# Performance work log

Measured on AMD Instinct MI355X. Metric: run time of the kernel, lower is better.

The kernel has to match this reference:

```python
import jax, jax.numpy as jnp
import numpy as np

BN_EPS = 1e-5

def conv1x1(x, w, b):
    # x: [B,C,H,W], w: [O,C], b: [O] -> [B,O,H,W]
    return jnp.einsum('bchw,oc->bohw', x, w) + b[None, :, None, None]

def setup_inputs() -> dict:
    key = jax.random.key(0)
    ks = jax.random.split(key, 12)
    B, C, H, W = 16, 256, 64, 32
    Ci = C // 2  # reduc_ratio = 2
    s_in = 1.0 / np.sqrt(C)
    s_ci = 1.0 / np.sqrt(Ci)
    return {
        'x':        jax.random.normal(ks[0], (B, C, H, W), jnp.float32),
        'w_theta':  jax.random.normal(ks[1], (Ci, C), jnp.float32) * s_in,
        'b_theta':  jax.random.normal(ks[2], (Ci,), jnp.float32) * 0.01,
        'w_phi':    jax.random.normal(ks[3], (Ci, C), jnp.float32) * s_in,
        'b_phi':    jax.random.normal(ks[4], (Ci,), jnp.float32) * 0.01,
        'w_g':      jax.random.normal(ks[5], (Ci, C), jnp.float32) * s_in,
        'b_g':      jax.random.normal(ks[6], (Ci,), jnp.float32) * 0.01,
        'w_out':    jax.random.normal(ks[7], (C, Ci), jnp.float32) * s_ci,
        'b_out':    jax.random.normal(ks[8], (C,), jnp.float32) * 0.01,
        'gamma':    jax.random.normal(ks[9], (C,), jnp.float32) * 0.1 + 1.0,
        'beta':     jax.random.normal(ks[10], (C,), jnp.float32) * 0.1,
        'run_mean': jax.random.normal(ks[11], (C,), jnp.float32) * 0.1,
        'run_var':  jax.random.uniform(jax.random.fold_in(key, 99), (C,), jnp.float32, 0.5, 1.5),
    }

def reference(x, w_theta, b_theta, w_phi, b_phi, w_g, b_g, w_out, b_out,
              gamma, beta, run_mean, run_var):
    B, C, H, W = x.shape
    Ci = w_theta.shape[0]
    N = H * W
    theta = conv1x1(x, w_theta, b_theta).reshape(B, Ci, N)  # [B,Ci,N]
    phi   = conv1x1(x, w_phi,   b_phi  ).reshape(B, Ci, N)  # [B,Ci,N]
    g     = conv1x1(x, w_g,     b_g    ).reshape(B, Ci, N)  # [B,Ci,N]
    # f = theta^T @ phi, normalized by N (no softmax)
    f = jnp.einsum('bcn,bcm->bnm', theta, phi) / N           # [B,N,N]
    # y = f @ g^T, back to channel-first layout
    y = jnp.einsum('bnm,bcm->bcn', f, g).reshape(B, Ci, H, W)
    w_y = conv1x1(y, w_out, b_out)                           # [B,C,H,W]
    inv = gamma / jnp.sqrt(run_var + BN_EPS)
    bn = w_y * inv[None, :, None, None] + (beta - run_mean * inv)[None, :, None, None]
    return bn + x
```

## Files before the change

kernel.cpp:

```cpp
#include <hip/hip_runtime.h>
#include <cstddef>
#include <cstdint>

typedef unsigned short ushort_t;
typedef short short8 __attribute__((ext_vector_type(8)));
typedef float f32x4 __attribute__((ext_vector_type(4)));

#define BB 16
#define CC 256
#define CI 128
#define NN 2048
#define BN_EPS 1e-5f
#define NCH 4

#define OFF_EH    0u
#define OFF_WGT   16384u
#define OFF_WFT   32768u
#define OFF_WTT   49152u
#define OFF_LH    65536u
#define OFF_RT    98304u
#define OFF_Q     131072u
#define OFF_W1    131328u
#define OFF_EG    131584u
#define OFF_BB2   131840u
#define OFF_BFBT  132096u
#define OFF_S     132112u
#define OFF_V1    136208u
#define OFF_V2    140304u
#define OFF_SQ    144400u
#define OFF_BIASP 144416u
#define OFF_GH    148512u
#define OFF_TH    672800u
#define OFF_PH    1197088u
#define OFF_XH    1721376u
#define OFF_XHT   5915680u
#define OFF_GP    10109984u
#define WS_FLOATS 14304288u

__device__ __forceinline__ ushort_t f2bf(float f) {
  unsigned int u = __float_as_uint(f);
  u += 0x7fffu + ((u >> 16) & 1u);
  return (ushort_t)(u >> 16);
}
__device__ __forceinline__ float bf2f(ushort_t h) {
  return __uint_as_float((unsigned int)h << 16);
}

__device__ __forceinline__ void gl_lds16(const void* gsrc, void* ldst) {
  __builtin_amdgcn_global_load_lds(
      (const __attribute__((address_space(1))) void*)gsrc,
      (__attribute__((address_space(3))) void*)ldst, 16, 0, 0);
}

__device__ __forceinline__ void mfma_core(
    const ushort_t* gA, size_t ldA, const ushort_t* gB, size_t ldB,
    int kIters, ushort_t* ldsA, ushort_t* ldsB, f32x4 acc[4][4]) {
  const int t = threadIdx.x;
  const int wave = t >> 6, lane = t & 63;
  const int wm = wave & 1, wn = wave >> 1;
  const int l15 = lane & 15, lhi = lane >> 4;

  for (int kt = 0; kt < kIters; ++kt) {
#pragma unroll
    for (int q = 0; q < 4; ++q) {
      int row = wave * 32 + q * 8 + (lane >> 3);
      int gs = (lane & 7) ^ (row & 7);
      gl_lds16(gA + (size_t)row * ldA + gs * 8, &ldsA[(wave * 4 + q) * 512]);
    }
#pragma unroll
    for (int q = 0; q < 4; ++q) {
      int row = wave * 32 + q * 8 + (lane >> 3);
      int gs = (lane & 7) ^ (row & 7);
      gl_lds16(gB + (size_t)row * ldB + gs * 8, &ldsB[(wave * 4 + q) * 512]);
    }
    __syncthreads();
#pragma unroll
    for (int ks = 0; ks < 2; ++ks) {
      short8 af[4], bf[4];
#pragma unroll
      for (int i = 0; i < 4; ++i) {
        int rowA = wm * 64 + i * 16 + l15;
        int grA = (4 * ks + lhi) ^ (rowA & 7);
        af[i] = *(const short8*)&ldsA[rowA * 64 + grA * 8];
        int rowB = wn * 64 + i * 16 + l15;
        int grB = (4 * ks + lhi) ^ (rowB & 7);
        bf[i] = *(const short8*)&ldsB[rowB * 64 + grB * 8];
      }
#pragma unroll
      for (int i = 0; i < 4; ++i)
#pragma unroll
        for (int j = 0; j < 4; ++j)
          acc[i][j] = __builtin_amdgcn_mfma_f32_16x16x32_bf16(
              af[i], bf[j], acc[i][j], 0, 0, 0);
    }
    __syncthreads();
    gA += 64; gB += 64;
  }
}

#define ACC_INIT(acc) \
  _Pragma("unroll") for (int i_ = 0; i_ < 4; ++i_) \
  _Pragma("unroll") for (int j_ = 0; j_ < 4; ++j_) \
  _Pragma("unroll") for (int e_ = 0; e_ < 4; ++e_) acc[i_][j_][e_] = 0.f;

__device__ __forceinline__ void store_bf16_D(
    f32x4 acc[4][4], ushort_t* D, int ldd, int m0, int n0) {
  int t = threadIdx.x, wave = t >> 6, lane = t & 63;
  int wm = wave & 1, wn = wave >> 1, l15 = lane & 15, lhi = lane >> 4;
#pragma unroll
  for (int i = 0; i < 4; ++i)
#pragma unroll
    for (int j = 0; j < 4; ++j)
#pragma unroll
      for (int r = 0; r < 4; ++r) {
        int a = m0 + wm * 64 + i * 16 + 4 * lhi + r;
        int bc = n0 + wn * 64 + j * 16 + l15;
        D[(size_t)a * ldd + bc] = f2bf(acc[i][j][r]);
      }
}

__global__ __launch_bounds__(256) void pack(
    const float* __restrict__ wg, const float* __restrict__ wp,
    const float* __restrict__ wt, const float* __restrict__ wout,
    const float* __restrict__ gamma, const float* __restrict__ run_var,
    const float* __restrict__ b_out, const float* __restrict__ beta,
    const float* __restrict__ run_mean,
    ushort_t* __restrict__ Eh, ushort_t* __restrict__ WgT,
    ushort_t* __restrict__ WfT, ushort_t* __restrict__ WtT,
    float* __restrict__ bias2) {
  int gid = blockIdx.x * 256 + threadIdx.x;
  if (gid < 4 * 32768) {
    int which = gid >> 15, idx = gid & 32767;
    int c = idx >> 7, j = idx & 127;
    if (which == 0) {
      float inv = gamma[c] * rsqrtf(run_var[c] + BN_EPS);
      Eh[idx] = f2bf(inv * (1.0f / (float)NN) * wout[idx]);
    } else {
      const float* src = (which == 1) ? wg : (which == 2) ? wp : wt;
      ushort_t* dst = (which == 1) ? WgT : (which == 2) ? WfT : WtT;
      dst[idx] = f2bf(src[(size_t)j * CC + c]);
    }
  } else if (gid < 4 * 32768 + CC) {
    int o = gid - 4 * 32768;
    float inv = gamma[o] * rsqrtf(run_var[o] + BN_EPS);
    bias2[o] = b_out[o] * inv + beta[o] - run_mean[o] * inv;
  }
}

__global__ __launch_bounds__(256) void pack2(
    const float* __restrict__ wp, const float* __restrict__ wt,
    const float* __restrict__ wout, const float* __restrict__ bt,
    const float* __restrict__ bp, const float* __restrict__ bg,
    const float* __restrict__ gamma, const float* __restrict__ run_var,
    float* __restrict__ q, float* __restrict__ w1, float* __restrict__ eg,
    float* __restrict__ bfbt) {
  int t = threadIdx.x;
  float aq = 0.f, aw = 0.f;
  for (int j = 0; j < CI; ++j) {
    aq += wp[(size_t)j * CC + t] * bt[j];
    aw += wt[(size_t)j * CC + t] * bp[j];
  }
  q[t] = aq; w1[t] = aw;
  float inv = gamma[t] * rsqrtf(run_var[t] + BN_EPS);
  float s2 = 0.f;
  for (int i = 0; i < CI; ++i) s2 += wout[(size_t)t * CI + i] * bg[i];
  eg[t] = inv * (1.0f / (float)NN) * s2;
  if (t == 0) {
    float d = 0.f;
    for (int j = 0; j < CI; ++j) d += bp[j] * bt[j];
    *bfbt = d;
  }
}

__global__ __launch_bounds__(256) void cast_x(
    const float* __restrict__ x, ushort_t* __restrict__ xhT,
    ushort_t* __restrict__ xh, float* __restrict__ s) {
  __shared__ float Xs[64][65];
  int n0 = blockIdx.x * 64, c0 = blockIdx.y * 64, b = blockIdx.z;
  int t = threadIdx.x;
  int tr = t >> 4, tc = (t & 15) * 4;
#pragma unroll
  for (int p = 0; p < 4; ++p) {
    int row = p * 16 + tr;
    float4 v = *(const float4*)&x[((size_t)b * CC + c0 + row) * NN + n0 + tc];
    Xs[row][tc] = v.x; Xs[row][tc + 1] = v.y; Xs[row][tc + 2] = v.z; Xs[row][tc + 3] = v.w;
  }
  __syncthreads();
#pragma unroll
  for (int p = 0; p < 4; ++p) {
    int j = p * 16 + tr;
    ushort4 hv;
    hv.x = f2bf(Xs[tc][j]); hv.y = f2bf(Xs[tc + 1][j]);
    hv.z = f2bf(Xs[tc + 2][j]); hv.w = f2bf(Xs[tc + 3][j]);
    *(ushort4*)&xhT[((size_t)b * NN + n0 + j) * CC + c0 + tc] = hv;
  }
  {
    int row = t >> 2, cg = (t & 3) * 16;
    size_t base = ((size_t)b * CC + c0 + row) * NN + n0 + cg;
#pragma unroll
    for (int e = 0; e < 4; ++e) {
      ushort4 hv;
      hv.x = f2bf(Xs[row][cg + 4 * e]);     hv.y = f2bf(Xs[row][cg + 4 * e + 1]);
      hv.z = f2bf(Xs[row][cg + 4 * e + 2]); hv.w = f2bf(Xs[row][cg + 4 * e + 3]);
      *(ushort4*)&xh[base + 4 * e] = hv;
    }
  }
  if (t < 64) {
    float p = 0.f;
    for (int j2 = 0; j2 < 64; ++j2) p += Xs[t][j2];
    atomicAdd(&s[(size_t)b * CC + c0 + t], p);
  }
}

__global__ __launch_bounds__(256) void gemm_k128(
    const ushort_t* __restrict__ A, const ushort_t* __restrict__ B,
    ushort_t* __restrict__ D) {
  __shared__ __align__(16) ushort_t As[8192], Bs[8192];
  int n0 = blockIdx.x * 128, m0 = blockIdx.y * 128;
  f32x4 acc[4][4]; ACC_INIT(acc);
  mfma_core(A + (size_t)m0 * 128, 128, B + (size_t)n0 * 128, 128, 2, As, Bs, acc);
  store_bf16_D(acc, D, CC, m0, n0);
}

__global__ __launch_bounds__(256) void k_G(
    const ushort_t* __restrict__ xh, float* __restrict__ G_part) {
  __shared__ __align__(16) ushort_t As[8192], Bs[8192];
  int ch = blockIdx.x, ij = blockIdx.y, b = blockIdx.z;
  int ti = ij >> 1, tj = ij & 1;
  f32x4 acc[4][4]; ACC_INIT(acc);
  mfma_core(xh + ((size_t)b * CC + ti * 128) * NN + ch * (NN / NCH), NN,
            xh + ((size_t)b * CC + tj * 128) * NN + ch * (NN / NCH), NN,
            (NN / NCH) / 64, As, Bs, acc);
  float* dst = G_part + ((size_t)ch * BB + b) * (CC * CC);
  int t = threadIdx.x, wave = t >> 6, lane = t & 63;
  int wm = wave & 1, wn = wave >> 1, l15 = lane & 15, lhi = lane >> 4;
#pragma unroll
  for (int i = 0; i < 4; ++i)
#pragma unroll
    for (int j = 0; j < 4; ++j)
#pragma unroll
      for (int r = 0; r < 4; ++r) {
        int a = ti * 128 + wm * 64 + i * 16 + 4 * lhi + r;
        int bc = tj * 128 + wn * 64 + j * 16 + l15;
        dst[(size_t)a * CC + bc] = acc[i][j][r];
      }
}

__global__ __launch_bounds__(256) void g_red(
    const float* __restrict__ G_part, ushort_t* __restrict__ Gh) {
  int b = blockIdx.y;
  int e = blockIdx.x * 256 + threadIdx.x;
  float v = 0.f;
#pragma unroll
  for (int c = 0; c < NCH; ++c)
    v += G_part[((size_t)c * BB + b) * (CC * CC) + e];
  Gh[(size_t)b * (CC * CC) + e] = f2bf(v);
}

__global__ __launch_bounds__(256) void k_s(
    const ushort_t* __restrict__ Lh, const ushort_t* __restrict__ Rt,
    const float* __restrict__ s, const float* __restrict__ q,
    float* __restrict__ v1, float* __restrict__ v2, float* __restrict__ sq) {
  __shared__ float sl[256], red[256];
  int b = blockIdx.x, t = threadIdx.x;
  sl[t] = s[(size_t)b * CC + t];
  __syncthreads();
  float a1 = 0.f, a2 = 0.f;
  for (int c = 0; c < CC; ++c) {
    a1 += bf2f(Lh[(size_t)t * CC + c]) * sl[c];
    a2 += bf2f(Rt[(size_t)t * CC + c]) * sl[c];
  }
  v1[(size_t)b * CC + t] = a1;
  v2[(size_t)b * CC + t] = a2;
  red[t] = sl[t] * q[t];
  __syncthreads();
  for (int st = 128; st > 0; st >>= 1) {
    if (t < st) red[t] += red[t + st];
    __syncthreads();
  }
  if (t == 0) sq[b] = red[0];
}

__global__ __launch_bounds__(256) void c1(
    const ushort_t* __restrict__ Lh, const ushort_t* __restrict__ Gh,
    ushort_t* __restrict__ Th) {
  __shared__ __align__(16) ushort_t As[8192], Bs[8192];
  int n0 = blockIdx.x * 128, m0 = blockIdx.y * 128, b = blockIdx.z;
  f32x4 acc[4][4]; ACC_INIT(acc);
  mfma_core(Lh + (size_t)m0 * CC, CC,
            Gh + (size_t)b * (CC * CC) + (size_t)n0 * CC, CC, 4, As, Bs, acc);
  store_bf16_D(acc, Th + (size_t)b * (CC * CC), CC, m0, n0);
}

__global__ __launch_bounds__(256) void c2(
    const ushort_t* __restrict__ Th, const ushort_t* __restrict__ Rt,
    const float* __restrict__ v1, const float* __restrict__ v2,
    const float* __restrict__ eg, const float* __restrict__ w1,
    ushort_t* __restrict__ Ph) {
  __shared__ __align__(16) ushort_t As[8192], Bs[8192];
  int n0 = blockIdx.x * 128, m0 = blockIdx.y * 128, b = blockIdx.z;
  f32x4 acc[4][4]; ACC_INIT(acc);
  mfma_core(Th + (size_t)b * (CC * CC) + (size_t)m0 * CC, CC,
            Rt + (size_t)n0 * CC, CC, 4, As, Bs, acc);
  ushort_t* D = Ph + (size_t)b * (CC * CC);
  int t = threadIdx.x, wave = t >> 6, lane = t & 63;
  int wm = wave & 1, wn = wave >> 1, l15 = lane & 15, lhi = lane >> 4;
#pragma unroll
  for (int i = 0; i < 4; ++i)
#pragma unroll
    for (int r = 0; r < 4; ++r) {
      int o = m0 + wm * 64 + i * 16 + 4 * lhi + r;
      float vo = v1[(size_t)b * CC + o] + (float)NN * eg[o];
      float eo = eg[o];
#pragma unroll
      for (int j = 0; j < 4; ++j) {
        int c = n0 + wn * 64 + j * 16 + l15;
        float val = acc[i][j][r] + eo * v2[(size_t)b * CC + c] + vo * w1[c];
        D[(size_t)o * CC + c] = f2bf(val);
      }
    }
}

__global__ __launch_bounds__(256) void k_bias(
    const ushort_t* __restrict__ Th, const float* __restrict__ q,
    const float* __restrict__ eg, const float* __restrict__ v1,
    const float* __restrict__ sq, const float* __restrict__ bfbt,
    const float* __restrict__ bias2, float* __restrict__ biasp) {
  int b = blockIdx.x, o = threadIdx.x;
  const ushort_t* Trow = Th + (size_t)b * (CC * CC) + (size_t)o * CC;
  float a = 0.f;
  for (int k = 0; k < CC; ++k) a += bf2f(Trow[k]) * q[k];
  biasp[(size_t)b * CC + o] =
      a + eg[o] * sq[b] + (v1[(size_t)b * CC + o] + (float)NN * eg[o]) * (*bfbt)
      + bias2[o];
}

__global__ __launch_bounds__(256) void k_out(
    const ushort_t* __restrict__ Ph, const ushort_t* __restrict__ xhT,
    const float* __restrict__ biasp, const float* __restrict__ x,
    float* __restrict__ out) {
  __shared__ __align__(16) ushort_t As[8192], Bs[8192];
  int n0 = blockIdx.x * 128, o0 = blockIdx.y * 128, b = blockIdx.z;
  f32x4 acc[4][4]; ACC_INIT(acc);
  mfma_core(Ph + (size_t)b * (CC * CC) + (size_t)o0 * CC, CC,
            xhT + ((size_t)b * NN + n0) * CC, CC, 4, As, Bs, acc);
  int t = threadIdx.x, wave = t >> 6, lane = t & 63;
  int wm = wave & 1, wn = wave >> 1, l15 = lane & 15, lhi = lane >> 4;
#pragma unroll
  for (int i = 0; i < 4; ++i)
#pragma unroll
    for (int r = 0; r < 4; ++r) {
      int o = o0 + wm * 64 + i * 16 + 4 * lhi + r;
      float bo = biasp[(size_t)b * CC + o];
#pragma unroll
      for (int j = 0; j < 4; ++j) {
        int n = n0 + wn * 64 + j * 16 + l15;
        size_t idx = ((size_t)b * CC + o) * NN + n;
        out[idx] = acc[i][j][r] + bo + x[idx];
      }
    }
}

extern "C" void kernel_launch(void* const* d_in, const int* in_sizes, int n_in,
                              void* d_out, int out_size, void* d_ws, size_t ws_size,
                              hipStream_t stream) {
  const float* x        = (const float*)d_in[0];
  const float* w_theta  = (const float*)d_in[1];
  const float* b_theta  = (const float*)d_in[2];
  const float* w_phi    = (const float*)d_in[3];
  const float* b_phi    = (const float*)d_in[4];
  const float* w_g      = (const float*)d_in[5];
  const float* b_g      = (const float*)d_in[6];
  const float* w_out    = (const float*)d_in[7];
  const float* b_out    = (const float*)d_in[8];
  const float* gamma    = (const float*)d_in[9];
  const float* beta     = (const float*)d_in[10];
  const float* run_mean = (const float*)d_in[11];
  const float* run_var  = (const float*)d_in[12];
  float* out = (float*)d_out;
  float* ws  = (float*)d_ws;

  if (ws_size < (size_t)WS_FLOATS * sizeof(float)) return;

  ushort_t* Eh   = (ushort_t*)(ws + OFF_EH);
  ushort_t* WgT  = (ushort_t*)(ws + OFF_WGT);
  ushort_t* WfT  = (ushort_t*)(ws + OFF_WFT);
  ushort_t* WtT  = (ushort_t*)(ws + OFF_WTT);
  ushort_t* Lh   = (ushort_t*)(ws + OFF_LH);
  ushort_t* Rt   = (ushort_t*)(ws + OFF_RT);
  float*    q    = ws + OFF_Q;
  float*    w1   = ws + OFF_W1;
  float*    eg   = ws + OFF_EG;
  float*    bias2= ws + OFF_BB2;
  float*    bfbt = ws + OFF_BFBT;
  float*    s    = ws + OFF_S;
  float*    v1   = ws + OFF_V1;
  float*    v2   = ws + OFF_V2;
  float*    sq   = ws + OFF_SQ;
  float*    biasp= ws + OFF_BIASP;
  ushort_t* Gh   = (ushort_t*)(ws + OFF_GH);
  ushort_t* Th   = (ushort_t*)(ws + OFF_TH);
  ushort_t* Ph   = (ushort_t*)(ws + OFF_PH);
  ushort_t* xh   = (ushort_t*)(ws + OFF_XH);
  ushort_t* xhT  = (ushort_t*)(ws + OFF_XHT);
  float*    Gp   = ws + OFF_GP;

  pack<<<dim3(513), 256, 0, stream>>>(w_g, w_phi, w_theta, w_out, gamma, run_var,
                                      b_out, beta, run_mean, Eh, WgT, WfT, WtT, bias2);
  pack2<<<dim3(1), 256, 0, stream>>>(w_phi, w_theta, w_out, b_theta, b_phi, b_g,
                                     gamma, run_var, q, w1, eg, bfbt);
  hipMemsetAsync(s, 0, (size_t)BB * CC * sizeof(float), stream);
  cast_x<<<dim3(NN / 64, CC / 64, BB), 256, 0, stream>>>(x, xhT, xh, s);
  gemm_k128<<<dim3(2, 2), 256, 0, stream>>>(Eh, WgT, Lh);
  gemm_k128<<<dim3(2, 2), 256, 0, stream>>>(WtT, WfT, Rt);
  k_G<<<dim3(NCH, 4, BB), 256, 0, stream>>>(xh, Gp);
  g_red<<<dim3(CC * CC / 256, BB), 256, 0, stream>>>(Gp, Gh);
  k_s<<<dim3(BB), 256, 0, stream>>>(Lh, Rt, s, q, v1, v2, sq);
  c1<<<dim3(2, 2, BB), 256, 0, stream>>>(Lh, Gh, Th);
  c2<<<dim3(2, 2, BB), 256, 0, stream>>>(Th, Rt, v1, v2, eg, w1, Ph);
  k_bias<<<dim3(BB), 256, 0, stream>>>(Th, q, eg, v1, sq, bfbt, bias2, biasp);
  k_out<<<dim3(NN / 128, CC / 128, BB), 256, 0, stream>>>(Ph, xhT, biasp, x, out);
}
```

Baseline: 207.1 us.

## Fuse prep and per-batch chain kernels, drop split-K, read bf16 residual

New measurement: 266.0 us. +28.4%, slower.

```diff
diff --git a/kernel.cpp b/kernel.cpp
--- a/kernel.cpp
+++ b/kernel.cpp
@@ -11,31 +11,22 @@
 #define CI 128
 #define NN 2048
 #define BN_EPS 1e-5f
-#define NCH 4
-
-#define OFF_EH    0u
-#define OFF_WGT   16384u
-#define OFF_WFT   32768u
-#define OFF_WTT   49152u
-#define OFF_LH    65536u
-#define OFF_RT    98304u
-#define OFF_Q     131072u
-#define OFF_W1    131328u
-#define OFF_EG    131584u
-#define OFF_BB2   131840u
-#define OFF_BFBT  132096u
-#define OFF_S     132112u
-#define OFF_V1    136208u
-#define OFF_V2    140304u
-#define OFF_SQ    144400u
-#define OFF_BIASP 144416u
-#define OFF_GH    148512u
-#define OFF_TH    672800u
-#define OFF_PH    1197088u
-#define OFF_XH    1721376u
-#define OFF_XHT   5915680u
-#define OFF_GP    10109984u
-#define WS_FLOATS 14304288u
+
+#define OFF_LH    0u
+#define OFF_RT    32768u
+#define OFF_Q     65536u
+#define OFF_W1    65792u
+#define OFF_EG    66048u
+#define OFF_BB2   66304u
+#define OFF_BFBT  66560u
+#define OFF_BIASP 66576u
+#define OFF_SS    70672u
+#define OFF_GH    74768u
+#define OFF_TH    599056u
+#define OFF_PH    1123344u
+#define OFF_XH    1647632u
+#define OFF_XHT   5841936u
+#define WS_FLOATS 10036240u
 
 __device__ __forceinline__ ushort_t f2bf(float f) {
   unsigned int u = __float_as_uint(f);
@@ -119,56 +110,68 @@
       }
 }
 
-__global__ __launch_bounds__(256) void pack(
-    const float* __restrict__ wg, const float* __restrict__ wp,
-    const float* __restrict__ wt, const float* __restrict__ wout,
-    const float* __restrict__ gamma, const float* __restrict__ run_var,
-    const float* __restrict__ b_out, const float* __restrict__ beta,
-    const float* __restrict__ run_mean,
-    ushort_t* __restrict__ Eh, ushort_t* __restrict__ WgT,
-    ushort_t* __restrict__ WfT, ushort_t* __restrict__ WtT,
-    float* __restrict__ bias2) {
-  int gid = blockIdx.x * 256 + threadIdx.x;
-  if (gid < 4 * 32768) {
-    int which = gid >> 15, idx = gid & 32767;
-    int c = idx >> 7, j = idx & 127;
-    if (which == 0) {
-      float inv = gamma[c] * rsqrtf(run_var[c] + BN_EPS);
-      Eh[idx] = f2bf(inv * (1.0f / (float)NN) * wout[idx]);
-    } else {
-      const float* src = (which == 1) ? wg : (which == 2) ? wp : wt;
-      ushort_t* dst = (which == 1) ? WgT : (which == 2) ? WfT : WtT;
-      dst[idx] = f2bf(src[(size_t)j * CC + c]);
-    }
-  } else if (gid < 4 * 32768 + CC) {
-    int o = gid - 4 * 32768;
-    float inv = gamma[o] * rsqrtf(run_var[o] + BN_EPS);
-    bias2[o] = b_out[o] * inv + beta[o] - run_mean[o] * inv;
-  }
-}
-
-__global__ __launch_bounds__(256) void pack2(
-    const float* __restrict__ wp, const float* __restrict__ wt,
-    const float* __restrict__ wout, const float* __restrict__ bt,
-    const float* __restrict__ bp, const float* __restrict__ bg,
-    const float* __restrict__ gamma, const float* __restrict__ run_var,
+__global__ __launch_bounds__(256) void prep(
+    const float* __restrict__ wt, const float* __restrict__ wp,
+    const float* __restrict__ wg, const float* __restrict__ wout,
+    const float* __restrict__ bt, const float* __restrict__ bp,
+    const float* __restrict__ bg, const float* __restrict__ gamma,
+    const float* __restrict__ beta, const float* __restrict__ run_mean,
+    const float* __restrict__ run_var, const float* __restrict__ b_out,
+    ushort_t* __restrict__ Lh, ushort_t* __restrict__ Rt,
     float* __restrict__ q, float* __restrict__ w1, float* __restrict__ eg,
-    float* __restrict__ bfbt) {
-  int t = threadIdx.x;
-  float aq = 0.f, aw = 0.f;
-  for (int j = 0; j < CI; ++j) {
-    aq += wp[(size_t)j * CC + t] * bt[j];
-    aw += wt[(size_t)j * CC + t] * bp[j];
-  }
-  q[t] = aq; w1[t] = aw;
-  float inv = gamma[t] * rsqrtf(run_var[t] + BN_EPS);
-  float s2 = 0.f;
-  for (int i = 0; i < CI; ++i) s2 += wout[(size_t)t * CI + i] * bg[i];
-  eg[t] = inv * (1.0f / (float)NN) * s2;
-  if (t == 0) {
-    float d = 0.f;
-    for (int j = 0; j < CI; ++j) d += bp[j] * bt[j];
-    *bfbt = d;
+    float* __restrict__ bias2, float* __restrict__ bfbt,
+    float* __restrict__ s) {
+  int blk = blockIdx.x, t = threadIdx.x;
+  if (blk < 16) {
+    int o = blk * 16 + (t >> 4);
+    int j0 = (t & 15) * 16;
+    float inv = gamma[o] * rsqrtf(run_var[o] + BN_EPS) * (1.0f / (float)NN);
+    float acc[16];
+#pragma unroll
+    for (int e = 0; e < 16; ++e) acc[e] = 0.f;
+    for (int k = 0; k < CI; ++k) {
+      float a = wout[(size_t)o * CI + k];
+      const float* wgr = &wg[(size_t)k * CC + j0];
+#pragma unroll
+      for (int e = 0; e < 16; ++e) acc[e] += a * wgr[e];
+    }
+#pragma unroll
+    for (int e = 0; e < 16; ++e)
+      Lh[(size_t)o * CC + j0 + e] = f2bf(inv * acc[e]);
+  } else if (blk < 32) {
+    int a = (blk - 16) * 16 + (t >> 4);
+    int b0 = (t & 15) * 16;
+    float acc[16];
+#pragma unroll
+    for (int e = 0; e < 16; ++e) acc[e] = 0.f;
+    for (int j = 0; j < CI; ++j) {
+      float av = wt[(size_t)j * CC + a];
+      const float* wpr = &wp[(size_t)j * CC + b0];
+#pragma unroll
+      for (int e = 0; e < 16; ++e) acc[e] += av * wpr[e];
+    }
+#pragma unroll
+    for (int e = 0; e < 16; ++e)
+      Rt[(size_t)a * CC + b0 + e] = f2bf(acc[e]);
+  } else {
+    float aq = 0.f, aw = 0.f;
+    for (int j = 0; j < CI; ++j) {
+      aq += wp[(size_t)j * CC + t] * bt[j];
+      aw += wt[(size_t)j * CC + t] * bp[j];
+    }
+    q[t] = aq; w1[t] = aw;
+    float inv = gamma[t] * rsqrtf(run_var[t] + BN_EPS);
+    float s2 = 0.f;
+    for (int i = 0; i < CI; ++i) s2 += wout[(size_t)t * CI + i] * bg[i];
+    eg[t] = inv * (1.0f / (float)NN) * s2;
+    bias2[t] = b_out[t] * inv + beta[t] - run_mean[t] * inv;
+    if (t == 0) {
+      float d = 0.f;
+      for (int j = 0; j < CI; ++j) d += bp[j] * bt[j];
+      *bfbt = d;
+    }
+#pragma unroll
+    for (int i = 0; i < BB; ++i) s[(size_t)i * CC + t] = 0.f;
   }
 }
 
@@ -212,137 +215,121 @@
   }
 }
 
-__global__ __launch_bounds__(256) void gemm_k128(
-    const ushort_t* __restrict__ A, const ushort_t* __restrict__ B,
-    ushort_t* __restrict__ D) {
+__global__ __launch_bounds__(256) void k_G(
+    const ushort_t* __restrict__ xh, ushort_t* __restrict__ Gh_all) {
   __shared__ __align__(16) ushort_t As[8192], Bs[8192];
-  int n0 = blockIdx.x * 128, m0 = blockIdx.y * 128;
-  f32x4 acc[4][4]; ACC_INIT(acc);
-  mfma_core(A + (size_t)m0 * 128, 128, B + (size_t)n0 * 128, 128, 2, As, Bs, acc);
-  store_bf16_D(acc, D, CC, m0, n0);
-}
-
-__global__ __launch_bounds__(256) void k_G(
-    const ushort_t* __restrict__ xh, float* __restrict__ G_part) {
-  __shared__ __align__(16) ushort_t As[8192], Bs[8192];
-  int ch = blockIdx.x, ij = blockIdx.y, b = blockIdx.z;
+  int ij = blockIdx.x, b = blockIdx.y;
   int ti = ij >> 1, tj = ij & 1;
   f32x4 acc[4][4]; ACC_INIT(acc);
-  mfma_core(xh + ((size_t)b * CC + ti * 128) * NN + ch * (NN / NCH), NN,
-            xh + ((size_t)b * CC + tj * 128) * NN + ch * (NN / NCH), NN,
-            (NN / NCH) / 64, As, Bs, acc);
-  float* dst = G_part + ((size_t)ch * BB + b) * (CC * CC);
-  int t = threadIdx.x, wave = t >> 6, lane = t & 63;
-  int wm = wave & 1, wn = wave >> 1, l15 = lane & 15, lhi = lane >> 4;
-#pragma unroll
-  for (int i = 0; i < 4; ++i)
-#pragma unroll
-    for (int j = 0; j < 4; ++j)
-#pragma unroll
-      for (int r = 0; r < 4; ++r) {
-        int a = ti * 128 + wm * 64 + i * 16 + 4 * lhi + r;
-        int bc = tj * 128 + wn * 64 + j * 16 + l15;
-        dst[(size_t)a * CC + bc] = acc[i][j][r];
-      }
-}
-
-__global__ __launch_bounds__(256) void g_red(
-    const float* __restrict__ G_part, ushort_t* __restrict__ Gh) {
-  int b = blockIdx.y;
-  int e = blockIdx.x * 256 + threadIdx.x;
-  float v = 0.f;
-#pragma unroll
-  for (int c = 0; c < NCH; ++c)
-    v += G_part[((size_t)c * BB + b) * (CC * CC) + e];
-  Gh[(size_t)b * (CC * CC) + e] = f2bf(v);
-}
-
-__global__ __launch_bounds__(256) void k_s(
-    const ushort_t* __restrict__ Lh, const ushort_t* __restrict__ Rt,
-    const float* __restrict__ s, const float* __restrict__ q,
-    float* __restrict__ v1, float* __restrict__ v2, float* __restrict__ sq) {
-  __shared__ float sl[256], red[256];
+  mfma_core(xh + ((size_t)b * CC + ti * 128) * NN, NN,
+            xh + ((size_t)b * CC + tj * 128) * NN, NN, NN / 64, As, Bs, acc);
+  store_bf16_D(acc, Gh_all + (size_t)b * (CC * CC), CC, ti * 128, tj * 128);
+}
+
+__global__ __launch_bounds__(256) void k_cc(
+    const float* __restrict__ s, const ushort_t* __restrict__ Lh,
+    const ushort_t* __restrict__ Rt, const ushort_t* __restrict__ Gh_all,
+    ushort_t* __restrict__ Th_all, ushort_t* __restrict__ Ph_all,
+    const float* __restrict__ q, const float* __restrict__ w1,
+    const float* __restrict__ eg, const float* __restrict__ bias2,
+    const float* __restrict__ bfbt, float* __restrict__ biasp) {
+  __shared__ __align__(16) ushort_t As[8192], Bs[8192];
+  __shared__ float sl[256], v1l[256], v2l[256], red[256];
+  __shared__ float ql[256], egl[256], w1l[256];
+  __shared__ float sql;
   int b = blockIdx.x, t = threadIdx.x;
+  const ushort_t* Gh = Gh_all + (size_t)b * (CC * CC);
+  ushort_t* Th = Th_all + (size_t)b * (CC * CC);
+  ushort_t* Ph = Ph_all + (size_t)b * (CC * CC);
+
   sl[t] = s[(size_t)b * CC + t];
-  __syncthreads();
-  float a1 = 0.f, a2 = 0.f;
-  for (int c = 0; c < CC; ++c) {
-    a1 += bf2f(Lh[(size_t)t * CC + c]) * sl[c];
-    a2 += bf2f(Rt[(size_t)t * CC + c]) * sl[c];
-  }
-  v1[(size_t)b * CC + t] = a1;
-  v2[(size_t)b * CC + t] = a2;
-  red[t] = sl[t] * q[t];
+  ql[t] = q[t]; egl[t] = eg[t]; w1l[t] = w1[t];
+  __syncthreads();
+
+  {
+    int rl = t >> 4, ch = t & 15;
+    for (int pass = 0; pass < 16; ++pass) {
+      int o = pass * 16 + rl;
+      float a1 = 0.f, a2 = 0.f;
+#pragma unroll
+      for (int e = 0; e < 16; ++e) {
+        float sv = sl[ch * 16 + e];
+        a1 += bf2f(Lh[(size_t)o * CC + ch * 16 + e]) * sv;
+        a2 += bf2f(Rt[(size_t)o * CC + ch * 16 + e]) * sv;
+      }
+#pragma unroll
+      for (int w = 8; w >= 1; w >>= 1) {
+        a1 += __shfl_xor(a1, w, 16);
+        a2 += __shfl_xor(a2, w, 16);
+      }
+      if (ch == 0) { v1l[o] = a1; v2l[o] = a2; }
+    }
+    red[t] = sl[t] * ql[t];
+  }
   __syncthreads();
   for (int st = 128; st > 0; st >>= 1) {
     if (t < st) red[t] += red[t + st];
     __syncthreads();
   }
-  if (t == 0) sq[b] = red[0];
-}
-
-__global__ __launch_bounds__(256) void c1(
-    const ushort_t* __restrict__ Lh, const ushort_t* __restrict__ Gh,
-    ushort_t* __restrict__ Th) {
-  __shared__ __align__(16) ushort_t As[8192], Bs[8192];
-  int n0 = blockIdx.x * 128, m0 = blockIdx.y * 128, b = blockIdx.z;
-  f32x4 acc[4][4]; ACC_INIT(acc);
-  mfma_core(Lh + (size_t)m0 * CC, CC,
-            Gh + (size_t)b * (CC * CC) + (size_t)n0 * CC, CC, 4, As, Bs, acc);
-  store_bf16_D(acc, Th + (size_t)b * (CC * CC), CC, m0, n0);
-}
-
-__global__ __launch_bounds__(256) void c2(
-    const ushort_t* __restrict__ Th, const ushort_t* __restrict__ Rt,
-    const float* __restrict__ v1, const float* __restrict__ v2,
-    const float* __restrict__ eg, const float* __restrict__ w1,
-    ushort_t* __restrict__ Ph) {
-  __shared__ __align__(16) ushort_t As[8192], Bs[8192];
-  int n0 = blockIdx.x * 128, m0 = blockIdx.y * 128, b = blockIdx.z;
-  f32x4 acc[4][4]; ACC_INIT(acc);
-  mfma_core(Th + (size_t)b * (CC * CC) + (size_t)m0 * CC, CC,
-            Rt + (size_t)n0 * CC, CC, 4, As, Bs, acc);
-  ushort_t* D = Ph + (size_t)b * (CC * CC);
-  int t = threadIdx.x, wave = t >> 6, lane = t & 63;
+  if (t == 0) sql = red[0];
+  __syncthreads();
+
+  for (int m0 = 0; m0 < CC; m0 += 128)
+    for (int n0 = 0; n0 < CC; n0 += 128) {
+      f32x4 acc[4][4]; ACC_INIT(acc);
+      mfma_core(Lh + (size_t)m0 * CC, CC, Gh + (size_t)n0 * CC, CC, 4, As, Bs, acc);
+      store_bf16_D(acc, Th, CC, m0, n0);
+    }
+  __syncthreads();
+
+  int wave = t >> 6, lane = t & 63;
   int wm = wave & 1, wn = wave >> 1, l15 = lane & 15, lhi = lane >> 4;
-#pragma unroll
-  for (int i = 0; i < 4; ++i)
-#pragma unroll
-    for (int r = 0; r < 4; ++r) {
-      int o = m0 + wm * 64 + i * 16 + 4 * lhi + r;
-      float vo = v1[(size_t)b * CC + o] + (float)NN * eg[o];
-      float eo = eg[o];
-#pragma unroll
-      for (int j = 0; j < 4; ++j) {
-        int c = n0 + wn * 64 + j * 16 + l15;
-        float val = acc[i][j][r] + eo * v2[(size_t)b * CC + c] + vo * w1[c];
-        D[(size_t)o * CC + c] = f2bf(val);
-      }
-    }
-}
-
-__global__ __launch_bounds__(256) void k_bias(
-    const ushort_t* __restrict__ Th, const float* __restrict__ q,
-    const float* __restrict__ eg, const float* __restrict__ v1,
-    const float* __restrict__ sq, const float* __restrict__ bfbt,
-    const float* __restrict__ bias2, float* __restrict__ biasp) {
-  int b = blockIdx.x, o = threadIdx.x;
-  const ushort_t* Trow = Th + (size_t)b * (CC * CC) + (size_t)o * CC;
-  float a = 0.f;
-  for (int k = 0; k < CC; ++k) a += bf2f(Trow[k]) * q[k];
-  biasp[(size_t)b * CC + o] =
-      a + eg[o] * sq[b] + (v1[(size_t)b * CC + o] + (float)NN * eg[o]) * (*bfbt)
-      + bias2[o];
+  for (int m0 = 0; m0 < CC; m0 += 128)
+    for (int n0 = 0; n0 < CC; n0 += 128) {
+      f32x4 acc[4][4]; ACC_INIT(acc);
+      mfma_core(Th + (size_t)m0 * CC, CC, Rt + (size_t)n0 * CC, CC, 4, As, Bs, acc);
+#pragma unroll
+      for (int i = 0; i < 4; ++i)
+#pragma unroll
+        for (int r = 0; r < 4; ++r) {
+          int o = m0 + wm * 64 + i * 16 + 4 * lhi + r;
+          float vo = v1l[o] + (float)NN * egl[o];
+          float eo = egl[o];
+#pragma unroll
+          for (int j = 0; j < 4; ++j) {
+            int c = n0 + wn * 64 + j * 16 + l15;
+            Ph[(size_t)o * CC + c] = f2bf(acc[i][j][r] + eo * v2l[c] + vo * w1l[c]);
+          }
+        }
+    }
+  __syncthreads();
+
+  {
+    float bf = *bfbt;
+    int rl = t >> 4, ch = t & 15;
+    for (int pass = 0; pass < 16; ++pass) {
+      int o = pass * 16 + rl;
+      float a = 0.f;
+#pragma unroll
+      for (int e = 0; e < 16; ++e)
+        a += bf2f(Th[(size_t)o * CC + ch * 16 + e]) * ql[ch * 16 + e];
+#pragma unroll
+      for (int w = 8; w >= 1; w >>= 1) a += __shfl_xor(a, w, 16);
+      if (ch == 0)
+        biasp[(size_t)b * CC + o] = a + egl[o] * sql +
+            (v1l[o] + (float)NN * egl[o]) * bf + bias2[o];
+    }
+  }
 }
 
 __global__ __launch_bounds__(256) void k_out(
-    const ushort_t* __restrict__ Ph, const ushort_t* __restrict__ xhT,
-    const float* __restrict__ biasp, const float* __restrict__ x,
+    const ushort_t* __restrict__ Ph_all, const ushort_t* __restrict__ xhT,
+    const ushort_t* __restrict__ xh, const float* __restrict__ biasp,
     float* __restrict__ out) {
   __shared__ __align__(16) ushort_t As[8192], Bs[8192];
   int n0 = blockIdx.x * 128, o0 = blockIdx.y * 128, b = blockIdx.z;
   f32x4 acc[4][4]; ACC_INIT(acc);
-  mfma_core(Ph + (size_t)b * (CC * CC) + (size_t)o0 * CC, CC,
+  mfma_core(Ph_all + (size_t)b * (CC * CC) + (size_t)o0 * CC, CC,
             xhT + ((size_t)b * NN + n0) * CC, CC, 4, As, Bs, acc);
   int t = threadIdx.x, wave = t >> 6, lane = t & 63;
   int wm = wave & 1, wn = wave >> 1, l15 = lane & 15, lhi = lane >> 4;
@@ -356,7 +343,7 @@
       for (int j = 0; j < 4; ++j) {
         int n = n0 + wn * 64 + j * 16 + l15;
         size_t idx = ((size_t)b * CC + o) * NN + n;
-        out[idx] = acc[i][j][r] + bo + x[idx];
+        out[idx] = acc[i][j][r] + bo + bf2f(xh[idx]);
       }
     }
 }
@@ -382,42 +369,27 @@
 
   if (ws_size < (size_t)WS_FLOATS * sizeof(float)) return;
 
-  ushort_t* Eh   = (ushort_t*)(ws + OFF_EH);
-  ushort_t* WgT  = (ushort_t*)(ws + OFF_WGT);
-  ushort_t* WfT  = (ushort_t*)(ws + OFF_WFT);
-  ushort_t* WtT  = (ushort_t*)(ws + OFF_WTT);
-  ushort_t* Lh   = (ushort_t*)(ws + OFF_LH);
-  ushort_t* Rt   = (ushort_t*)(ws + OFF_RT);
-  float*    q    = ws + OFF_Q;
-  float*    w1   = ws + OFF_W1;
-  float*    eg   = ws + OFF_EG;
-  float*    bias2= ws + OFF_BB2;
-  float*    bfbt = ws + OFF_BFBT;
-  float*    s    = ws + OFF_S;
-  float*    v1   = ws + OFF_V1;
-  float*    v2   = ws + OFF_V2;
-  float*    sq   = ws + OFF_SQ;
-  float*    biasp= ws + OFF_BIASP;
-  ushort_t* Gh   = (ushort_t*)(ws + OFF_GH);
-  ushort_t* Th   = (ushort_t*)(ws + OFF_TH);
-  ushort_t* Ph   = (ushort_t*)(ws + OFF_PH);
-  ushort_t* xh   = (ushort_t*)(ws + OFF_XH);
-  ushort_t* xhT  = (ushort_t*)(ws + OFF_XHT);
-  float*    Gp   = ws + OFF_GP;
-
-  pack<<<dim3(513), 256, 0, stream>>>(w_g, w_phi, w_theta, w_out, gamma, run_var,
-                                      b_out, beta, run_mean, Eh, WgT, WfT, WtT, bias2);
-  pack2<<<dim3(1), 256, 0, stream>>>(w_phi, w_theta, w_out, b_theta, b_phi, b_g,
-                                     gamma, run_var, q, w1, eg, bfbt);
-  hipMemsetAsync(s, 0, (size_t)BB * CC * sizeof(float), stream);
+  ushort_t* Lh    = (ushort_t*)(ws + OFF_LH);
+  ushort_t* Rt    = (ushort_t*)(ws + OFF_RT);
+  float*    q     = ws + OFF_Q;
+  float*    w1    = ws + OFF_W1;
+  float*    eg    = ws + OFF_EG;
+  float*    bias2 = ws + OFF_BB2;
+  float*    bfbt  = ws + OFF_BFBT;
+  float*    biasp = ws + OFF_BIASP;
+  float*    s     = ws + OFF_SS;
+  ushort_t* Gh    = (ushort_t*)(ws + OFF_GH);
+  ushort_t* Th    = (ushort_t*)(ws + OFF_TH);
+  ushort_t* Ph    = (ushort_t*)(ws + OFF_PH);
+  ushort_t* xh    = (ushort_t*)(ws + OFF_XH);
+  ushort_t* xhT   = (ushort_t*)(ws + OFF_XHT);
+
+  prep<<<dim3(33), 256, 0, stream>>>(w_theta, w_phi, w_g, w_out,
+      b_theta, b_phi, b_g, gamma, beta, run_mean, run_var, b_out,
+      Lh, Rt, q, w1, eg, bias2, bfbt, s);
   cast_x<<<dim3(NN / 64, CC / 64, BB), 256, 0, stream>>>(x, xhT, xh, s);
-  gemm_k128<<<dim3(2, 2), 256, 0, stream>>>(Eh, WgT, Lh);
-  gemm_k128<<<dim3(2, 2), 256, 0, stream>>>(WtT, WfT, Rt);
-  k_G<<<dim3(NCH, 4, BB), 256, 0, stream>>>(xh, Gp);
-  g_red<<<dim3(CC * CC / 256, BB), 256, 0, stream>>>(Gp, Gh);
-  k_s<<<dim3(BB), 256, 0, stream>>>(Lh, Rt, s, q, v1, v2, sq);
-  c1<<<dim3(2, 2, BB), 256, 0, stream>>>(Lh, Gh, Th);
-  c2<<<dim3(2, 2, BB), 256, 0, stream>>>(Th, Rt, v1, v2, eg, w1, Ph);
-  k_bias<<<dim3(BB), 256, 0, stream>>>(Th, q, eg, v1, sq, bfbt, bias2, biasp);
-  k_out<<<dim3(NN / 128, CC / 128, BB), 256, 0, stream>>>(Ph, xhT, biasp, x, out);
-}
+  k_G<<<dim3(4, BB), 256, 0, stream>>>(xh, Gh);
+  k_cc<<<dim3(BB), 256, 0, stream>>>(s, Lh, Rt, Gh, Th, Ph,
+                                     q, w1, eg, bias2, bfbt, biasp);
+  k_out<<<dim3(NN / 128, CC / 128, BB), 256, 0, stream>>>(Ph, xhT, xh, biasp, out);
+}
```
